# Kernel tuning notes

Measured on AMD Instinct MI355X. Metric: run time of the kernel, lower is better.

Reference implementation:

```python
import jax, jax.numpy as jnp
import numpy as np

S, B, E, H = 2048, 4, 512, 8
D = E // H

# --- Brevitas-style per-tensor fake quantization with straight-through estimator ---

def fq_s8(x):
    """Int8ActPerTensorFloat / Int8WeightPerTensorFloat: symmetric per-tensor abs-max."""
    qmax = 127.0
    scale = jnp.maximum(jnp.max(jnp.abs(x)), 1e-8) / qmax
    q = jnp.clip(jnp.round(x / scale), -128.0, qmax)
    return x + jax.lax.stop_gradient(scale * q - x), scale


def fq_u8(x):
    """Uint8ActPerTensorFloat for attention weights (softmax output, >=0)."""
    qmax = 255.0
    scale = jnp.maximum(jnp.max(x), 1e-8) / qmax
    q = jnp.clip(jnp.round(x / scale), 0.0, qmax)
    return x + jax.lax.stop_gradient(scale * q - x)


def fq_b32(b, scale):
    """Int32Bias: bias quantized with scale = input_scale * weight_scale."""
    qmax = 2.0 ** 31 - 1.0
    q = jnp.clip(jnp.round(b / scale), -qmax, qmax)
    return b + jax.lax.stop_gradient(scale * q - b)


def setup_inputs() -> dict:
    key = jax.random.key(0)
    ks = jax.random.split(key, 9)
    w = lambda k: jax.random.normal(k, (E, E), jnp.float32) * 0.02
    b = lambda k: jax.random.normal(k, (E,), jnp.float32) * 0.02
    return {
        "x": jax.random.normal(ks[0], (S, B, E), jnp.float32),
        "Wq": w(ks[1]), "Wk": w(ks[2]), "Wv": w(ks[3]),
        "bq": b(ks[4]), "bk": b(ks[5]), "bv": b(ks[6]),
        "Wo": w(ks[7]), "bo": b(ks[8]),
    }


def reference(x, Wq, Wk, Wv, bq, bk, bv, Wo, bo):
    # inputQuant (QuantIdentity, int8)
    xq, _ = fq_s8(x)
    # in_proj input quant (int8, per-tensor)
    xi, s_in = fq_s8(xq)

    def proj(W, b_):
        Wf, s_w = fq_s8(W)                    # int8 weight quant
        bf = fq_b32(b_, s_in * s_w)           # int32 bias quant
        return jnp.einsum('sbe,fe->sbf', xi, Wf) + bf

    q = proj(Wq, bq)  # [S,B,E]
    k = proj(Wk, bk)
    v = proj(Wv, bv)

    # split heads: [S,B,E] -> [B,H,S,D]
    heads = lambda t: t.reshape(S, B, H, D).transpose(1, 2, 0, 3)
    q, k, v = heads(q), heads(k), heads(v)

    qs, _ = fq_s8(q / jnp.sqrt(jnp.float32(D)))   # q_scaled_quant (int8)
    kt, _ = fq_s8(k)                              # k_transposed_quant (int8)
    scores = jnp.einsum('bhqd,bhkd->bhqk', qs, kt)  # [B,H,S,S]
    attn = fq_u8(jax.nn.softmax(scores, axis=-1))   # attn_output_weights_quant (uint8)
    vq, _ = fq_s8(v)                                # v_quant (int8)

    ctx = jnp.einsum('bhqk,bhkd->bhqd', attn, vq)   # [B,H,S,D]
    ctx = ctx.transpose(2, 0, 1, 3).reshape(S, B, E)  # back to [S,B,E]

    ci, s_c = fq_s8(ctx)                            # out_proj_input_quant
    Wof, s_wo = fq_s8(Wo)                           # out_proj_weight_quant
    bof = fq_b32(bo, s_c * s_wo)                    # out_proj_bias_quant
    y = jnp.einsum('sbe,fe->sbf', ci, Wof) + bof
    yq, _ = fq_s8(y)                                # out_proj_output_quant
    return yq
```

## Files before the change

### kernel.cpp

```cpp
#include <hip/hip_runtime.h>

constexpr int cS = 2048, cB = 4, cE = 512, cH = 8, cD = 64;
constexpr int cSB = cS * cB;
constexpr int cBH = cB * cH;
constexpr int cN  = cSB * cE;

typedef __bf16 v8bf  __attribute__((ext_vector_type(8)));
typedef float  f32x4 __attribute__((ext_vector_type(4)));

constexpr float cLOG2E = 1.4426950408889634f;


__device__ __forceinline__ unsigned short q2bf(float f) {
  return (unsigned short)(__float_as_uint(f) >> 16);
}
__device__ __forceinline__ float clip8(float t) { return fminf(fmaxf(t, -128.f), 127.f); }
__device__ __forceinline__ float wave_max(float v) {
#pragma unroll
  for (int o = 32; o > 0; o >>= 1) v = fmaxf(v, __shfl_down(v, o));
  return v;
}

__device__ __forceinline__ void stage8k(const unsigned short* __restrict__ gsrc,
                                        unsigned short* lds, int tid) {
  int w = tid >> 6;
#pragma unroll
  for (int is = 0; is < 2; ++is) {
    int c = is * 256 + tid;
    int cp = (c & ~7) | ((c & 7) ^ ((c >> 3) & 7));
    const char* g = (const char*)gsrc + (size_t)cp * 16;
    char* l = (char*)lds + (size_t)(is * 4096 + w * 1024);
    __builtin_amdgcn_global_load_lds(
        (const __attribute__((address_space(1))) unsigned int*)g,
        (__attribute__((address_space(3))) unsigned int*)l, 16, 0, 0);
  }
}
__device__ __forceinline__ v8bf lds_frag(const unsigned short* tile, int row, int chunk) {
  int sc = chunk ^ (row & 7);
  return *(const v8bf*)((const char*)tile + row * 128 + sc * 16);
}

__global__ void absmax_kernel(const float* __restrict__ p, int n4, unsigned* slot) {
  int tid = blockIdx.x * blockDim.x + threadIdx.x, stride = gridDim.x * blockDim.x;
  float m = 0.f;
  for (int i = tid; i < n4; i += stride) {
    float4 v = ((const float4*)p)[i];
    m = fmaxf(m, fmaxf(fmaxf(fabsf(v.x), fabsf(v.y)), fmaxf(fabsf(v.z), fabsf(v.w))));
  }
  m = wave_max(m);
  __shared__ float sm[4];
  int lane = threadIdx.x & 63, wid = threadIdx.x >> 6;
  if (lane == 0) sm[wid] = m;
  __syncthreads();
  if (threadIdx.x == 0) {
    float mm = sm[0];
    for (int w = 1; w < (int)blockDim.x / 64; ++w) mm = fmaxf(mm, sm[w]);
    atomicMax(slot, __float_as_uint(mm));
  }
}

__global__ void absmax4_kernel(const float* __restrict__ w0, const float* __restrict__ w1,
                               const float* __restrict__ w2, const float* __restrict__ w3,
                               int n4, unsigned* slots) {
  int y = blockIdx.y;
  const float* p = (y == 0) ? w0 : (y == 1) ? w1 : (y == 2) ? w2 : w3;
  int tid = blockIdx.x * blockDim.x + threadIdx.x, stride = gridDim.x * blockDim.x;
  float m = 0.f;
  for (int i = tid; i < n4; i += stride) {
    float4 v = ((const float4*)p)[i];
    m = fmaxf(m, fmaxf(fmaxf(fabsf(v.x), fabsf(v.y)), fmaxf(fabsf(v.z), fabsf(v.w))));
  }
  m = wave_max(m);
  __shared__ float sm[4];
  int lane = threadIdx.x & 63, wid = threadIdx.x >> 6;
  if (lane == 0) sm[wid] = m;
  __syncthreads();
  if (threadIdx.x == 0) {
    float mm = fmaxf(fmaxf(sm[0], sm[1]), fmaxf(sm[2], sm[3]));
    atomicMax(slots + y, __float_as_uint(mm));
  }
}

__global__ void scales_kernel(float* st, int stage) {
  if (stage == 0) {
    float s0 = fmaxf(st[0], 1e-8f) / 127.f;
    st[11] = s0;
    float mxq = s0 * 127.f;
    st[12] = fmaxf(mxq, 1e-8f) / 127.f;
    for (int i = 0; i < 4; ++i) st[13 + i] = fmaxf(st[1 + i], 1e-8f) / 127.f;
  } else if (stage == 1) {
    st[17] = fmaxf(st[5] * 0.125f, 1e-8f) / 127.f;
    st[18] = fmaxf(st[6], 1e-8f) / 127.f;
    st[19] = fmaxf(st[7], 1e-8f) / 127.f;
    st[25] = st[17] * st[18];
    st[26] = st[25] * cLOG2E;
  } else if (stage == 2) {
    float sa = fmaxf(st[8], 1e-8f) / 255.f;
    st[20] = sa; st[21] = 1.f / sa; st[22] = sa * st[19];
  } else if (stage == 3) {
    st[23] = fmaxf(st[9], 1e-8f) / 127.f;
  } else {
    st[24] = fmaxf(st[10], 1e-8f) / 127.f;
  }
}

__global__ void quant_x_kernel(const float* __restrict__ x, unsigned short* __restrict__ xq,
                               const float* st, int n4) {
  float s0 = st[11], si = st[12];
  int tid = blockIdx.x * blockDim.x + threadIdx.x, stride = gridDim.x * blockDim.x;
  for (int i = tid; i < n4; i += stride) {
    float4 v = ((const float4*)x)[i];
    ushort4 o; float t;
    t = s0 * clip8(rintf(v.x / s0)); o.x = q2bf(clip8(rintf(t / si)));
    t = s0 * clip8(rintf(v.y / s0)); o.y = q2bf(clip8(rintf(t / si)));
    t = s0 * clip8(rintf(v.z / s0)); o.z = q2bf(clip8(rintf(t / si)));
    t = s0 * clip8(rintf(v.w / s0)); o.w = q2bf(clip8(rintf(t / si)));
    ((ushort4*)xq)[i] = o;
  }
}

__global__ void quant_w4_kernel(const float* __restrict__ w0, const float* __restrict__ w1,
                                const float* __restrict__ w2, const float* __restrict__ w3,
                                unsigned short* __restrict__ outbase, int n4, const float* st) {
  int y = blockIdx.y;
  const float* in = (y == 0) ? w0 : (y == 1) ? w1 : (y == 2) ? w2 : w3;
  unsigned short* outp = outbase + (size_t)y * cE * cE;
  float s = st[13 + y];
  int tid = blockIdx.x * blockDim.x + threadIdx.x, stride = gridDim.x * blockDim.x;
  for (int i = tid; i < n4; i += stride) {
    float4 v = ((const float4*)in)[i];
    ushort4 o;
    o.x = q2bf(clip8(rintf(v.x / s)));
    o.y = q2bf(clip8(rintf(v.y / s)));
    o.z = q2bf(clip8(rintf(v.z / s)));
    o.w = q2bf(clip8(rintf(v.w / s)));
    ((ushort4*)outp)[i] = o;
  }
}

__global__ void quant_s8_kernel(const float* __restrict__ in, unsigned short* __restrict__ outp,
                                int n4, const float* st, int slot, float premul) {
  float s = st[slot];
  int tid = blockIdx.x * blockDim.x + threadIdx.x, stride = gridDim.x * blockDim.x;
  for (int i = tid; i < n4; i += stride) {
    float4 v = ((const float4*)in)[i];
    ushort4 o;
    o.x = q2bf(clip8(rintf(v.x * premul / s)));
    o.y = q2bf(clip8(rintf(v.y * premul / s)));
    o.z = q2bf(clip8(rintf(v.z * premul / s)));
    o.w = q2bf(clip8(rintf(v.w * premul / s)));
    ((ushort4*)outp)[i] = o;
  }
}

__global__ void quant_qk_kernel(const float* __restrict__ qf, unsigned short* __restrict__ qsb,
                                int n4, const float* st) {
  int y = blockIdx.y;
  const float* in = qf + (size_t)y * cN;
  unsigned short* outp = qsb + (size_t)y * cN;
  float s = st[17 + y];
  float premul = y ? 1.0f : 0.125f;
  int tid = blockIdx.x * blockDim.x + threadIdx.x, stride = gridDim.x * blockDim.x;
  for (int i = tid; i < n4; i += stride) {
    float4 v = ((const float4*)in)[i];
    ushort4 o;
    o.x = q2bf(clip8(rintf(v.x * premul / s)));
    o.y = q2bf(clip8(rintf(v.y * premul / s)));
    o.z = q2bf(clip8(rintf(v.z * premul / s)));
    o.w = q2bf(clip8(rintf(v.w * premul / s)));
    ((ushort4*)outp)[i] = o;
  }
}

__global__ void bias3_kernel(const float* __restrict__ b0, const float* __restrict__ b1,
                             const float* __restrict__ b2, float* __restrict__ bdst,
                             const float* st) {
  int y = blockIdx.y;
  const float* bsrc = (y == 0) ? b0 : (y == 1) ? b1 : b2;
  int f = blockIdx.x * blockDim.x + threadIdx.x;
  if (f < cE) {
    float s = st[12] * st[13 + y];
    bdst[y * cE + f] = s * rintf(bsrc[f] / s);
  }
}

__global__ void bias_kernel(const float* __restrict__ bsrc, float* __restrict__ bdst,
                            const float* st, int slot_in, int slot_w) {
  int f = blockIdx.x * blockDim.x + threadIdx.x;
  if (f < cE) {
    float s = st[slot_in] * st[slot_w];
    bdst[f] = s * rintf(bsrc[f] / s);
  }
}

__global__ __launch_bounds__(256) void quant_vT_kernel(const float* __restrict__ v,
                                                       unsigned short* __restrict__ vT,
                                                       const float* st) {
  __shared__ unsigned short tile[64][65];
  int bh = blockIdx.y, bx = blockIdx.x, s0 = bx * 64;
  float sv = st[19];
  int td = threadIdx.x & 63, tr = threadIdx.x >> 6;
  for (int r = tr; r < 64; r += 4)
    tile[r][td] = q2bf(clip8(rintf(v[((size_t)bh * cS + s0 + r) * cD + td] / sv)));
  __syncthreads();
  for (int r = tr; r < 64; r += 4)
    vT[((size_t)(bh * 32 + bx) * 64 + r) * 64 + td] = tile[td][r];
}

__global__ void final_quant_kernel(float* __restrict__ y, const float* st, int n4) {
  float s = st[24];
  int tid = blockIdx.x * blockDim.x + threadIdx.x, stride = gridDim.x * blockDim.x;
  for (int i = tid; i < n4; i += stride) {
    float4 v = ((float4*)y)[i];
    v.x = s * clip8(rintf(v.x / s)); v.y = s * clip8(rintf(v.y / s));
    v.z = s * clip8(rintf(v.z / s)); v.w = s * clip8(rintf(v.w / s));
    ((float4*)y)[i] = v;
  }
}

template <int OUTMODE>
__global__ __launch_bounds__(256) void gemm_kernel(const unsigned short* __restrict__ A,
                                                   const unsigned short* __restrict__ Wb,
                                                   const float* __restrict__ bias,
                                                   float* __restrict__ out, const float* st,
                                                   int slot_in, int slot_w, unsigned* amax_slot) {
  int wid = threadIdx.x >> 6, lane = threadIdx.x & 63;
  int wm = wid >> 1, wn = wid & 1;
  int row0 = blockIdx.x * 64 + wm * 32;
  int col0 = blockIdx.y * 64 + wn * 32;
  int lr = lane & 15, lk = (lane >> 4) * 8;
  f32x4 acc[2][2] = {};
  const unsigned short* a0p = A + (size_t)(row0 + lr) * cE + lk;
  const unsigned short* a1p = A + (size_t)(row0 + 16 + lr) * cE + lk;
  const unsigned short* b0p = Wb + (size_t)(col0 + lr) * cE + lk;
  const unsigned short* b1p = Wb + (size_t)(col0 + 16 + lr) * cE + lk;
  for (int e0 = 0; e0 < cE; e0 += 32) {
    v8bf a0 = *(const v8bf*)(a0p + e0), a1 = *(const v8bf*)(a1p + e0);
    v8bf b0 = *(const v8bf*)(b0p + e0), b1 = *(const v8bf*)(b1p + e0);
    acc[0][0] = __builtin_amdgcn_mfma_f32_16x16x32_bf16(a0, b0, acc[0][0], 0, 0, 0);
    acc[0][1] = __builtin_amdgcn_mfma_f32_16x16x32_bf16(a0, b1, acc[0][1], 0, 0, 0);
    acc[1][0] = __builtin_amdgcn_mfma_f32_16x16x32_bf16(a1, b0, acc[1][0], 0, 0, 0);
    acc[1][1] = __builtin_amdgcn_mfma_f32_16x16x32_bf16(a1, b1, acc[1][1], 0, 0, 0);
  }
  float scale = st[slot_in] * st[slot_w];
  float lmax = 0.f;
#pragma unroll
  for (int mi = 0; mi < 2; ++mi)
#pragma unroll
    for (int ni = 0; ni < 2; ++ni)
#pragma unroll
      for (int r = 0; r < 4; ++r) {
        int row = row0 + mi * 16 + (lane >> 4) * 4 + r;
        int col = col0 + ni * 16 + lr;
        float val = scale * acc[mi][ni][r] + bias[col];
        lmax = fmaxf(lmax, fabsf(val));
        if (OUTMODE == 0) {
          int s = row >> 2, bb = row & 3, h = col >> 6, d = col & 63;
          out[(((size_t)(bb * cH + h)) * cS + s) * cD + d] = val;
        } else {
          out[(size_t)row * cE + col] = val;
        }
      }
  lmax = wave_max(lmax);
  if (lane == 0) atomicMax(amax_slot, __float_as_uint(lmax));
}

__global__ __launch_bounds__(256) void attn_pass1_kernel(const unsigned short* __restrict__ qs,
                                                         const unsigned short* __restrict__ ks,
                                                         float* __restrict__ marr,
                                                         float* __restrict__ izarr,
                                                         const float* st, unsigned* maxiz_slot) {
  __shared__ __align__(16) unsigned short kbuf[2][64][64];
  int tid = threadIdx.x;
  int bh = blockIdx.y;
  int wid = tid >> 6, lane = tid & 63;
  int lr = lane & 15, g = lane >> 4, lk = g * 8;
  int r0 = blockIdx.x * 128 + wid * 32;
  float sscale2 = st[26];
  v8bf aq0[2], aq1[2];
#pragma unroll
  for (int qg = 0; qg < 2; ++qg) {
    const unsigned short* qp = qs + ((size_t)bh * cS + r0 + qg * 16 + lr) * cD + lk;
    aq0[qg] = *(const v8bf*)qp; aq1[qg] = *(const v8bf*)(qp + 32);
  }
  const unsigned short* Kb = ks + (size_t)bh * cS * cD;

  stage8k(Kb, &kbuf[0][0][0], tid);
  __syncthreads();
  float pm[2] = {-1e30f, -1e30f}, zs[2] = {0.f, 0.f};
  int buf = 0;
  for (int t = 0; t < 32; ++t) {
    if (t < 31) stage8k(Kb + (size_t)(t + 1) * 4096, &kbuf[buf ^ 1][0][0], tid);
    const unsigned short* Kt = &kbuf[buf][0][0];
    f32x4 s4[2][4];
#pragma unroll
    for (int jc = 0; jc < 4; ++jc) {
      v8bf k0 = lds_frag(Kt, jc * 16 + lr, g);
      v8bf k1 = lds_frag(Kt, jc * 16 + lr, g + 4);
#pragma unroll
      for (int qg = 0; qg < 2; ++qg) {
        f32x4 z = {0.f, 0.f, 0.f, 0.f};
        z = __builtin_amdgcn_mfma_f32_16x16x32_bf16(k0, aq0[qg], z, 0, 0, 0);
        z = __builtin_amdgcn_mfma_f32_16x16x32_bf16(k1, aq1[qg], z, 0, 0, 0);
        s4[qg][jc] = z;
      }
    }
#pragma unroll
    for (int qg = 0; qg < 2; ++qg) {
      float tv[16];
#pragma unroll
      for (int jc = 0; jc < 4; ++jc)
#pragma unroll
        for (int r = 0; r < 4; ++r) tv[jc * 4 + r] = s4[qg][jc][r] * sscale2;
      float tm = tv[0];
#pragma unroll
      for (int i = 1; i < 16; ++i) tm = fmaxf(tm, tv[i]);
      float nm = fmaxf(pm[qg], tm);
      float acc = zs[qg] * __builtin_amdgcn_exp2f(pm[qg] - nm);
#pragma unroll
      for (int i = 0; i < 16; ++i) acc += __builtin_amdgcn_exp2f(tv[i] - nm);
      zs[qg] = acc; pm[qg] = nm;
    }
    __syncthreads();
    buf ^= 1;
  }
  float wm_l = 0.f;
#pragma unroll
  for (int qg = 0; qg < 2; ++qg) {
    float m = pm[qg], z = zs[qg];
#pragma unroll
    for (int o = 16; o < 64; o <<= 1) {
      float mo = __shfl_xor(m, o);
      float zo = __shfl_xor(z, o);
      float nm = fmaxf(m, mo);
      z = z * __builtin_amdgcn_exp2f(m - nm) + zo * __builtin_amdgcn_exp2f(mo - nm);
      m = nm;
    }
    float iz = 1.0f / z;
    if (g == 0) {
      marr[bh * cS + r0 + qg * 16 + lr] = m;
      izarr[bh * cS + r0 + qg * 16 + lr] = iz;
    }
    wm_l = fmaxf(wm_l, iz);
  }
  float wmax = wave_max(wm_l);
  if (lane == 0) atomicMax(maxiz_slot, __float_as_uint(wmax));
}

__global__ __launch_bounds__(256) void attn_pass2_kernel(
    const unsigned short* __restrict__ qs, const unsigned short* __restrict__ ks,
    const unsigned short* __restrict__ vT, const float* __restrict__ marr,
    const float* __restrict__ izarr, float* __restrict__ ctx, const float* st,
    unsigned* amax_slot) {
  __shared__ __align__(16) unsigned short kbuf[2][64][64];
  __shared__ __align__(16) unsigned short vbuf[2][64][64];
  __shared__ __align__(16) unsigned short plds[4][2][16][88];
  int tid = threadIdx.x;
  int bh = blockIdx.y, b = bh >> 3, h = bh & 7;
  int wid = tid >> 6, lane = tid & 63;
  int lr = lane & 15, g = lane >> 4, lk = g * 8;
  int r0 = blockIdx.x * 128 + wid * 32;
  float sscale2 = st[26], isa = st[21], cscale = st[22];
  v8bf aq0[2], aq1[2];
  float m2[2], fac[2];
#pragma unroll
  for (int qg = 0; qg < 2; ++qg) {
    const unsigned short* qp = qs + ((size_t)bh * cS + r0 + qg * 16 + lr) * cD + lk;
    aq0[qg] = *(const v8bf*)qp; aq1[qg] = *(const v8bf*)(qp + 32);
    m2[qg] = marr[bh * cS + r0 + qg * 16 + lr];
    fac[qg] = izarr[bh * cS + r0 + qg * 16 + lr] * isa;
  }
  const unsigned short* Kb = ks + (size_t)bh * cS * cD;
  const unsigned short* Vb = vT + (size_t)bh * 32 * 4096;
  f32x4 cacc[2][4] = {};

  stage8k(Kb, &kbuf[0][0][0], tid);
  stage8k(Vb, &vbuf[0][0][0], tid);
  __syncthreads();
  int buf = 0;
  for (int t = 0; t < 32; ++t) {
    if (t < 31) {
      stage8k(Kb + (size_t)(t + 1) * 4096, &kbuf[buf ^ 1][0][0], tid);
      stage8k(Vb + (size_t)(t + 1) * 4096, &vbuf[buf ^ 1][0][0], tid);
    }
    const unsigned short* Kt = &kbuf[buf][0][0];
    const unsigned short* Vt = &vbuf[buf][0][0];
#pragma unroll
    for (int jc = 0; jc < 4; ++jc) {
      v8bf k0 = lds_frag(Kt, jc * 16 + lr, g);
      v8bf k1 = lds_frag(Kt, jc * 16 + lr, g + 4);
#pragma unroll
      for (int qg = 0; qg < 2; ++qg) {
        f32x4 z = {0.f, 0.f, 0.f, 0.f};
        z = __builtin_amdgcn_mfma_f32_16x16x32_bf16(k0, aq0[qg], z, 0, 0, 0);
        z = __builtin_amdgcn_mfma_f32_16x16x32_bf16(k1, aq1[qg], z, 0, 0, 0);
        float a0 = fminf(rintf(__builtin_amdgcn_exp2f(__builtin_fmaf(z[0], sscale2, -m2[qg])) * fac[qg]), 255.f);
        float a1 = fminf(rintf(__builtin_amdgcn_exp2f(__builtin_fmaf(z[1], sscale2, -m2[qg])) * fac[qg]), 255.f);
        float a2 = fminf(rintf(__builtin_amdgcn_exp2f(__builtin_fmaf(z[2], sscale2, -m2[qg])) * fac[qg]), 255.f);
        float a3 = fminf(rintf(__builtin_amdgcn_exp2f(__builtin_fmaf(z[3], sscale2, -m2[qg])) * fac[qg]), 255.f);
        uint2 pw;
        pw.x = (__float_as_uint(a0) >> 16) | (__float_as_uint(a1) & 0xFFFF0000u);
        pw.y = (__float_as_uint(a2) >> 16) | (__float_as_uint(a3) & 0xFFFF0000u);
        *(uint2*)&plds[wid][qg][lr][jc * 16 + g * 4] = pw;
      }
    }
    v8bf ap0[2], ap1[2];
#pragma unroll
    for (int qg = 0; qg < 2; ++qg) {
      ap0[qg] = *(const v8bf*)&plds[wid][qg][lr][lk];
      ap1[qg] = *(const v8bf*)&plds[wid][qg][lr][32 + lk];
    }
#pragma unroll
    for (int dt = 0; dt < 4; ++dt) {
      v8bf v0 = lds_frag(Vt, dt * 16 + lr, g);
      v8bf v1 = lds_frag(Vt, dt * 16 + lr, g + 4);
#pragma unroll
      for (int qg = 0; qg < 2; ++qg) {
        cacc[qg][dt] = __builtin_amdgcn_mfma_f32_16x16x32_bf16(ap0[qg], v0, cacc[qg][dt], 0, 0, 0);
        cacc[qg][dt] = __builtin_amdgcn_mfma_f32_16x16x32_bf16(ap1[qg], v1, cacc[qg][dt], 0, 0, 0);
      }
    }
    __syncthreads();
    buf ^= 1;
  }
  float lmax = 0.f;
#pragma unroll
  for (int qg = 0; qg < 2; ++qg)
#pragma unroll
    for (int dt = 0; dt < 4; ++dt)
#pragma unroll
      for (int r = 0; r < 4; ++r) {
        int qrow = r0 + qg * 16 + g * 4 + r;
        int d = dt * 16 + lr;
        float val = cscale * cacc[qg][dt][r];
        lmax = fmaxf(lmax, fabsf(val));
        ctx[((size_t)qrow * cB + b) * cE + h * cD + d] = val;
      }
  lmax = wave_max(lmax);
  if (lane == 0) atomicMax(amax_slot, __float_as_uint(lmax));
}

extern "C" void kernel_launch(void* const* d_in, const int* in_sizes, int n_in, void* d_out,
                              int out_size, void* d_ws, size_t ws_size, hipStream_t stream) {
  (void)in_sizes; (void)n_in; (void)out_size; (void)ws_size;
  const float* x  = (const float*)d_in[0];
  const float* Wq = (const float*)d_in[1];
  const float* Wk = (const float*)d_in[2];
  const float* Wv = (const float*)d_in[3];
  const float* bq = (const float*)d_in[4];
  const float* bk = (const float*)d_in[5];
  const float* bv = (const float*)d_in[6];
  const float* Wo = (const float*)d_in[7];
  const float* bo = (const float*)d_in[8];
  float* out = (float*)d_out;

  char* ws = (char*)d_ws;
  size_t off = 0;
  auto alloc = [&](size_t bytes) { size_t o = off; off += (bytes + 255) & ~(size_t)255; return o; };
  float* st = (float*)(ws + alloc(64 * 4));
  unsigned short* xq  = (unsigned short*)(ws + alloc((size_t)cN * 2));
  unsigned short* wbq = (unsigned short*)(ws + alloc((size_t)cE * cE * 2));
  unsigned short* wbk = (unsigned short*)(ws + alloc((size_t)cE * cE * 2));
  unsigned short* wbv = (unsigned short*)(ws + alloc((size_t)cE * cE * 2));
  unsigned short* wbo = (unsigned short*)(ws + alloc((size_t)cE * cE * 2));
  float* bfq = (float*)(ws + alloc(cE * 4));
  float* bfk = (float*)(ws + alloc(cE * 4));
  float* bfv = (float*)(ws + alloc(cE * 4));
  float* bfo = (float*)(ws + alloc(cE * 4));
  float* qf = (float*)(ws + alloc((size_t)cN * 4));
  float* kf = (float*)(ws + alloc((size_t)cN * 4));
  float* vf = (float*)(ws + alloc((size_t)cN * 4));
  unsigned short* qsb = (unsigned short*)(ws + alloc((size_t)cN * 2));
  unsigned short* ksb = (unsigned short*)(ws + alloc((size_t)cN * 2));
  unsigned short* vTb = (unsigned short*)(ws + alloc((size_t)cN * 2));
  float* marr  = (float*)(ws + alloc((size_t)cBH * cS * 4));
  float* izarr = (float*)(ws + alloc((size_t)cBH * cS * 4));
  float* ctxf = qf;
  unsigned short* cib = (unsigned short*)kf;

  int n4 = cN / 4;
  int nw4 = cE * cE / 4;
  hipMemsetAsync(st, 0, 256, stream);
  absmax_kernel<<<1024, 256, 0, stream>>>(x, n4, (unsigned*)(st + 0));
  absmax4_kernel<<<dim3(64, 4), 256, 0, stream>>>(Wq, Wk, Wv, Wo, nw4, (unsigned*)(st + 1));
  scales_kernel<<<1, 1, 0, stream>>>(st, 0);
  quant_x_kernel<<<1024, 256, 0, stream>>>(x, xq, st, n4);
  quant_w4_kernel<<<dim3(64, 4), 256, 0, stream>>>(Wq, Wk, Wv, Wo, wbq, nw4, st);
  bias3_kernel<<<dim3(2, 3), 256, 0, stream>>>(bq, bk, bv, bfq, st);
  gemm_kernel<0><<<dim3(cSB / 64, cE / 64), 256, 0, stream>>>(xq, wbq, bfq, qf, st, 12, 13, (unsigned*)(st + 5));
  gemm_kernel<0><<<dim3(cSB / 64, cE / 64), 256, 0, stream>>>(xq, wbk, bfk, kf, st, 12, 14, (unsigned*)(st + 6));
  gemm_kernel<0><<<dim3(cSB / 64, cE / 64), 256, 0, stream>>>(xq, wbv, bfv, vf, st, 12, 15, (unsigned*)(st + 7));
  scales_kernel<<<1, 1, 0, stream>>>(st, 1);
  quant_qk_kernel<<<dim3(512, 2), 256, 0, stream>>>(qf, qsb, n4, st);
  quant_vT_kernel<<<dim3(cS / 64, cBH), 256, 0, stream>>>(vf, vTb, st);
  attn_pass1_kernel<<<dim3(cS / 128, cBH), 256, 0, stream>>>(qsb, ksb, marr, izarr, st, (unsigned*)(st + 8));
  scales_kernel<<<1, 1, 0, stream>>>(st, 2);
  attn_pass2_kernel<<<dim3(cS / 128, cBH), 256, 0, stream>>>(qsb, ksb, vTb, marr, izarr, ctxf, st, (unsigned*)(st + 9));
  scales_kernel<<<1, 1, 0, stream>>>(st, 3);
  quant_s8_kernel<<<1024, 256, 0, stream>>>(ctxf, cib, n4, st, 23, 1.0f);
  bias_kernel<<<2, 256, 0, stream>>>(bo, bfo, st, 23, 16);
  gemm_kernel<1><<<dim3(cSB / 64, cE / 64), 256, 0, stream>>>(cib, wbo, bfo, out, st, 23, 16, (unsigned*)(st + 10));
  scales_kernel<<<1, 1, 0, stream>>>(st, 4);
  final_quant_kernel<<<1024, 256, 0, stream>>>(out, st, n4);
}
```

Measured before the change: 535.0 us.

## Fuse QKV projections into one GEMM launch with LDS staging and drop scale kernels

Removes the five single-thread scales kernels and instead recomputes each quantization scale inline from the raw absmax slots inside every consumer kernel. It also merges the three Q/K/V projection GEMMs into one 24-column-block launch. The GEMM is rewritten to double-buffer swizzled 64x64 A/B tiles in LDS via global_load_lds instead of reading fragments straight from global memory. The aim is to cut launch count and serialization and to improve operand reuse in the GEMMs. The cost is a little redundant scalar math per thread and more LDS use. The fused launch relies on the K and V output buffers lying contiguously after qf, and the bias and weight buffers lying contiguously too.

```diff
diff --git a/kernel.cpp b/kernel.cpp
--- a/kernel.cpp
+++ b/kernel.cpp
@@ -15,6 +15,7 @@
   return (unsigned short)(__float_as_uint(f) >> 16);
 }
 __device__ __forceinline__ float clip8(float t) { return fminf(fmaxf(t, -128.f), 127.f); }
+__device__ __forceinline__ float sc127(float amax) { return fmaxf(amax, 1e-8f) / 127.f; }
 __device__ __forceinline__ float wave_max(float v) {
 #pragma unroll
   for (int o = 32; o > 0; o >>= 1) v = fmaxf(v, __shfl_down(v, o));
@@ -29,6 +30,21 @@
     int c = is * 256 + tid;
     int cp = (c & ~7) | ((c & 7) ^ ((c >> 3) & 7));
     const char* g = (const char*)gsrc + (size_t)cp * 16;
+    char* l = (char*)lds + (size_t)(is * 4096 + w * 1024);
+    __builtin_amdgcn_global_load_lds(
+        (const __attribute__((address_space(1))) unsigned int*)g,
+        (__attribute__((address_space(3))) unsigned int*)l, 16, 0, 0);
+  }
+}
+__device__ __forceinline__ void stage_rows(const unsigned short* __restrict__ g0,
+                                           unsigned short* lds, int tid) {
+  int w = tid >> 6;
+#pragma unroll
+  for (int is = 0; is < 2; ++is) {
+    int c = is * 256 + tid;
+    int row = c >> 3;
+    int kc = (c & 7) ^ (row & 7);
+    const char* g = (const char*)(g0 + (size_t)row * cE + kc * 8);
     char* l = (char*)lds + (size_t)(is * 4096 + w * 1024);
     __builtin_amdgcn_global_load_lds(
         (const __attribute__((address_space(1))) unsigned int*)g,
@@ -81,32 +97,10 @@
   }
 }
 
-__global__ void scales_kernel(float* st, int stage) {
-  if (stage == 0) {
-    float s0 = fmaxf(st[0], 1e-8f) / 127.f;
-    st[11] = s0;
-    float mxq = s0 * 127.f;
-    st[12] = fmaxf(mxq, 1e-8f) / 127.f;
-    for (int i = 0; i < 4; ++i) st[13 + i] = fmaxf(st[1 + i], 1e-8f) / 127.f;
-  } else if (stage == 1) {
-    st[17] = fmaxf(st[5] * 0.125f, 1e-8f) / 127.f;
-    st[18] = fmaxf(st[6], 1e-8f) / 127.f;
-    st[19] = fmaxf(st[7], 1e-8f) / 127.f;
-    st[25] = st[17] * st[18];
-    st[26] = st[25] * cLOG2E;
-  } else if (stage == 2) {
-    float sa = fmaxf(st[8], 1e-8f) / 255.f;
-    st[20] = sa; st[21] = 1.f / sa; st[22] = sa * st[19];
-  } else if (stage == 3) {
-    st[23] = fmaxf(st[9], 1e-8f) / 127.f;
-  } else {
-    st[24] = fmaxf(st[10], 1e-8f) / 127.f;
-  }
-}
-
 __global__ void quant_x_kernel(const float* __restrict__ x, unsigned short* __restrict__ xq,
                                const float* st, int n4) {
-  float s0 = st[11], si = st[12];
+  float s0 = sc127(st[0]);
+  float si = fmaxf(s0 * 127.f, 1e-8f) / 127.f;
   int tid = blockIdx.x * blockDim.x + threadIdx.x, stride = gridDim.x * blockDim.x;
   for (int i = tid; i < n4; i += stride) {
     float4 v = ((const float4*)x)[i];
@@ -125,7 +119,7 @@
   int y = blockIdx.y;
   const float* in = (y == 0) ? w0 : (y == 1) ? w1 : (y == 2) ? w2 : w3;
   unsigned short* outp = outbase + (size_t)y * cE * cE;
-  float s = st[13 + y];
+  float s = sc127(st[1 + y]);
   int tid = blockIdx.x * blockDim.x + threadIdx.x, stride = gridDim.x * blockDim.x;
   for (int i = tid; i < n4; i += stride) {
     float4 v = ((const float4*)in)[i];
@@ -138,9 +132,28 @@
   }
 }
 
-__global__ void quant_s8_kernel(const float* __restrict__ in, unsigned short* __restrict__ outp,
-                                int n4, const float* st, int slot, float premul) {
-  float s = st[slot];
+__global__ void quant_ctx_kernel(const float* __restrict__ in, unsigned short* __restrict__ outp,
+                                 int n4, const float* st) {
+  float s = sc127(st[9]);
+  int tid = blockIdx.x * blockDim.x + threadIdx.x, stride = gridDim.x * blockDim.x;
+  for (int i = tid; i < n4; i += stride) {
+    float4 v = ((const float4*)in)[i];
+    ushort4 o;
+    o.x = q2bf(clip8(rintf(v.x / s)));
+    o.y = q2bf(clip8(rintf(v.y / s)));
+    o.z = q2bf(clip8(rintf(v.z / s)));
+    o.w = q2bf(clip8(rintf(v.w / s)));
+    ((ushort4*)outp)[i] = o;
+  }
+}
+
+__global__ void quant_qk_kernel(const float* __restrict__ qf, unsigned short* __restrict__ qsb,
+                                int n4, const float* st) {
+  int y = blockIdx.y;
+  const float* in = qf + (size_t)y * cN;
+  unsigned short* outp = qsb + (size_t)y * cN;
+  float s = y ? sc127(st[6]) : (fmaxf(st[5] * 0.125f, 1e-8f) / 127.f);
+  float premul = y ? 1.0f : 0.125f;
   int tid = blockIdx.x * blockDim.x + threadIdx.x, stride = gridDim.x * blockDim.x;
   for (int i = tid; i < n4; i += stride) {
     float4 v = ((const float4*)in)[i];
@@ -153,25 +166,6 @@
   }
 }
 
-__global__ void quant_qk_kernel(const float* __restrict__ qf, unsigned short* __restrict__ qsb,
-                                int n4, const float* st) {
-  int y = blockIdx.y;
-  const float* in = qf + (size_t)y * cN;
-  unsigned short* outp = qsb + (size_t)y * cN;
-  float s = st[17 + y];
-  float premul = y ? 1.0f : 0.125f;
-  int tid = blockIdx.x * blockDim.x + threadIdx.x, stride = gridDim.x * blockDim.x;
-  for (int i = tid; i < n4; i += stride) {
-    float4 v = ((const float4*)in)[i];
-    ushort4 o;
-    o.x = q2bf(clip8(rintf(v.x * premul / s)));
-    o.y = q2bf(clip8(rintf(v.y * premul / s)));
-    o.z = q2bf(clip8(rintf(v.z * premul / s)));
-    o.w = q2bf(clip8(rintf(v.w * premul / s)));
-    ((ushort4*)outp)[i] = o;
-  }
-}
-
 __global__ void bias3_kernel(const float* __restrict__ b0, const float* __restrict__ b1,
                              const float* __restrict__ b2, float* __restrict__ bdst,
                              const float* st) {
@@ -179,16 +173,18 @@
   const float* bsrc = (y == 0) ? b0 : (y == 1) ? b1 : b2;
   int f = blockIdx.x * blockDim.x + threadIdx.x;
   if (f < cE) {
-    float s = st[12] * st[13 + y];
+    float s0 = sc127(st[0]);
+    float si = fmaxf(s0 * 127.f, 1e-8f) / 127.f;
+    float s = si * sc127(st[1 + y]);
     bdst[y * cE + f] = s * rintf(bsrc[f] / s);
   }
 }
 
-__global__ void bias_kernel(const float* __restrict__ bsrc, float* __restrict__ bdst,
-                            const float* st, int slot_in, int slot_w) {
+__global__ void bias_o_kernel(const float* __restrict__ bsrc, float* __restrict__ bdst,
+                              const float* st) {
   int f = blockIdx.x * blockDim.x + threadIdx.x;
   if (f < cE) {
-    float s = st[slot_in] * st[slot_w];
+    float s = sc127(st[9]) * sc127(st[4]);
     bdst[f] = s * rintf(bsrc[f] / s);
   }
 }
@@ -198,7 +194,7 @@
                                                        const float* st) {
   __shared__ unsigned short tile[64][65];
   int bh = blockIdx.y, bx = blockIdx.x, s0 = bx * 64;
-  float sv = st[19];
+  float sv = sc127(st[7]);
   int td = threadIdx.x & 63, tr = threadIdx.x >> 6;
   for (int r = tr; r < 64; r += 4)
     tile[r][td] = q2bf(clip8(rintf(v[((size_t)bh * cS + s0 + r) * cD + td] / sv)));
@@ -208,7 +204,7 @@
 }
 
 __global__ void final_quant_kernel(float* __restrict__ y, const float* st, int n4) {
-  float s = st[24];
+  float s = sc127(st[10]);
   int tid = blockIdx.x * blockDim.x + threadIdx.x, stride = gridDim.x * blockDim.x;
   for (int i = tid; i < n4; i += stride) {
     float4 v = ((float4*)y)[i];
@@ -218,31 +214,67 @@
   }
 }
 
-template <int OUTMODE>
+template <int MODE>
 __global__ __launch_bounds__(256) void gemm_kernel(const unsigned short* __restrict__ A,
-                                                   const unsigned short* __restrict__ Wb,
-                                                   const float* __restrict__ bias,
-                                                   float* __restrict__ out, const float* st,
-                                                   int slot_in, int slot_w, unsigned* amax_slot) {
-  int wid = threadIdx.x >> 6, lane = threadIdx.x & 63;
+                                                   const unsigned short* __restrict__ Wbase,
+                                                   const float* __restrict__ biasbase,
+                                                   float* __restrict__ outbase, const float* st,
+                                                   unsigned* amax_base) {
+  __shared__ __align__(16) unsigned short abuf[2][64][64];
+  __shared__ __align__(16) unsigned short bbuf[2][64][64];
+  int tid = threadIdx.x, wid = tid >> 6, lane = tid & 63;
   int wm = wid >> 1, wn = wid & 1;
-  int row0 = blockIdx.x * 64 + wm * 32;
-  int col0 = blockIdx.y * 64 + wn * 32;
-  int lr = lane & 15, lk = (lane >> 4) * 8;
+  int lr = lane & 15, g = lane >> 4;
+  int row0 = blockIdx.x * 64;
+  int wsel = (MODE == 0) ? (blockIdx.y >> 3) : 0;
+  int col0 = (MODE == 0) ? ((blockIdx.y & 7) * 64) : (blockIdx.y * 64);
+
+  float scale;
+  float* out;
+  const float* bias;
+  unsigned* amax_slot;
+  if (MODE == 0) {
+    float s0 = sc127(st[0]);
+    float si = fmaxf(s0 * 127.f, 1e-8f) / 127.f;
+    scale = si * sc127(st[1 + wsel]);
+    out = outbase + (size_t)wsel * cN;
+    bias = biasbase + wsel * cE;
+    amax_slot = amax_base + wsel;
+  } else {
+    scale = sc127(st[9]) * sc127(st[4]);
+    out = outbase;
+    bias = biasbase;
+    amax_slot = amax_base;
+  }
+  const unsigned short* Ab = A + (size_t)row0 * cE;
+  const unsigned short* Bb = Wbase + (size_t)wsel * cE * cE + (size_t)col0 * cE;
+
+  stage_rows(Ab, &abuf[0][0][0], tid);
+  stage_rows(Bb, &bbuf[0][0][0], tid);
+  __syncthreads();
   f32x4 acc[2][2] = {};
-  const unsigned short* a0p = A + (size_t)(row0 + lr) * cE + lk;
-  const unsigned short* a1p = A + (size_t)(row0 + 16 + lr) * cE + lk;
-  const unsigned short* b0p = Wb + (size_t)(col0 + lr) * cE + lk;
-  const unsigned short* b1p = Wb + (size_t)(col0 + 16 + lr) * cE + lk;
-  for (int e0 = 0; e0 < cE; e0 += 32) {
-    v8bf a0 = *(const v8bf*)(a0p + e0), a1 = *(const v8bf*)(a1p + e0);
-    v8bf b0 = *(const v8bf*)(b0p + e0), b1 = *(const v8bf*)(b1p + e0);
-    acc[0][0] = __builtin_amdgcn_mfma_f32_16x16x32_bf16(a0, b0, acc[0][0], 0, 0, 0);
-    acc[0][1] = __builtin_amdgcn_mfma_f32_16x16x32_bf16(a0, b1, acc[0][1], 0, 0, 0);
-    acc[1][0] = __builtin_amdgcn_mfma_f32_16x16x32_bf16(a1, b0, acc[1][0], 0, 0, 0);
-    acc[1][1] = __builtin_amdgcn_mfma_f32_16x16x32_bf16(a1, b1, acc[1][1], 0, 0, 0);
-  }
-  float scale = st[slot_in] * st[slot_w];
+  int buf = 0;
+  for (int kt = 0; kt < 8; ++kt) {
+    if (kt < 7) {
+      stage_rows(Ab + (kt + 1) * 64, &abuf[buf ^ 1][0][0], tid);
+      stage_rows(Bb + (kt + 1) * 64, &bbuf[buf ^ 1][0][0], tid);
+    }
+    const unsigned short* At = &abuf[buf][0][0];
+    const unsigned short* Bt = &bbuf[buf][0][0];
+#pragma unroll
+    for (int e = 0; e < 2; ++e) {
+      v8bf a0 = lds_frag(At, wm * 32 + lr, e * 4 + g);
+      v8bf a1 = lds_frag(At, wm * 32 + 16 + lr, e * 4 + g);
+      v8bf b0 = lds_frag(Bt, wn * 32 + lr, e * 4 + g);
+      v8bf b1 = lds_frag(Bt, wn * 32 + 16 + lr, e * 4 + g);
+      acc[0][0] = __builtin_amdgcn_mfma_f32_16x16x32_bf16(a0, b0, acc[0][0], 0, 0, 0);
+      acc[0][1] = __builtin_amdgcn_mfma_f32_16x16x32_bf16(a0, b1, acc[0][1], 0, 0, 0);
+      acc[1][0] = __builtin_amdgcn_mfma_f32_16x16x32_bf16(a1, b0, acc[1][0], 0, 0, 0);
+      acc[1][1] = __builtin_amdgcn_mfma_f32_16x16x32_bf16(a1, b1, acc[1][1], 0, 0, 0);
+    }
+    __syncthreads();
+    buf ^= 1;
+  }
   float lmax = 0.f;
 #pragma unroll
   for (int mi = 0; mi < 2; ++mi)
@@ -250,11 +282,11 @@
     for (int ni = 0; ni < 2; ++ni)
 #pragma unroll
       for (int r = 0; r < 4; ++r) {
-        int row = row0 + mi * 16 + (lane >> 4) * 4 + r;
-        int col = col0 + ni * 16 + lr;
+        int row = row0 + wm * 32 + mi * 16 + g * 4 + r;
+        int col = col0 + wn * 32 + ni * 16 + lr;
         float val = scale * acc[mi][ni][r] + bias[col];
         lmax = fmaxf(lmax, fabsf(val));
-        if (OUTMODE == 0) {
+        if (MODE == 0) {
           int s = row >> 2, bb = row & 3, h = col >> 6, d = col & 63;
           out[(((size_t)(bb * cH + h)) * cS + s) * cD + d] = val;
         } else {
@@ -276,7 +308,9 @@
   int wid = tid >> 6, lane = tid & 63;
   int lr = lane & 15, g = lane >> 4, lk = g * 8;
   int r0 = blockIdx.x * 128 + wid * 32;
-  float sscale2 = st[26];
+  float sq = fmaxf(st[5] * 0.125f, 1e-8f) / 127.f;
+  float sk = sc127(st[6]);
+  float sscale2 = (sq * sk) * cLOG2E;
   v8bf aq0[2], aq1[2];
 #pragma unroll
   for (int qg = 0; qg < 2; ++qg) {
@@ -360,7 +394,12 @@
   int wid = tid >> 6, lane = tid & 63;
   int lr = lane & 15, g = lane >> 4, lk = g * 8;
   int r0 = blockIdx.x * 128 + wid * 32;
-  float sscale2 = st[26], isa = st[21], cscale = st[22];
+  float sq = fmaxf(st[5] * 0.125f, 1e-8f) / 127.f;
+  float sk = sc127(st[6]);
+  float sscale2 = (sq * sk) * cLOG2E;
+  float sa = fmaxf(st[8], 1e-8f) / 255.f;
+  float isa = 1.f / sa;
+  float cscale = sa * sc127(st[7]);
   v8bf aq0[2], aq1[2];
   float m2[2], fac[2];
 #pragma unroll
@@ -480,26 +519,20 @@
 
   int n4 = cN / 4;
   int nw4 = cE * cE / 4;
+  (void)kf; (void)vf; (void)bfk; (void)bfv;
   hipMemsetAsync(st, 0, 256, stream);
   absmax_kernel<<<1024, 256, 0, stream>>>(x, n4, (unsigned*)(st + 0));
   absmax4_kernel<<<dim3(64, 4), 256, 0, stream>>>(Wq, Wk, Wv, Wo, nw4, (unsigned*)(st + 1));
-  scales_kernel<<<1, 1, 0, stream>>>(st, 0);
   quant_x_kernel<<<1024, 256, 0, stream>>>(x, xq, st, n4);
   quant_w4_kernel<<<dim3(64, 4), 256, 0, stream>>>(Wq, Wk, Wv, Wo, wbq, nw4, st);
   bias3_kernel<<<dim3(2, 3), 256, 0, stream>>>(bq, bk, bv, bfq, st);
-  gemm_kernel<0><<<dim3(cSB / 64, cE / 64), 256, 0, stream>>>(xq, wbq, bfq, qf, st, 12, 13, (unsigned*)(st + 5));
-  gemm_kernel<0><<<dim3(cSB / 64, cE / 64), 256, 0, stream>>>(xq, wbk, bfk, kf, st, 12, 14, (unsigned*)(st + 6));
-  gemm_kernel<0><<<dim3(cSB / 64, cE / 64), 256, 0, stream>>>(xq, wbv, bfv, vf, st, 12, 15, (unsigned*)(st + 7));
-  scales_kernel<<<1, 1, 0, stream>>>(st, 1);
+  gemm_kernel<0><<<dim3(cSB / 64, 24), 256, 0, stream>>>(xq, wbq, bfq, qf, st, (unsigned*)(st + 5));
   quant_qk_kernel<<<dim3(512, 2), 256, 0, stream>>>(qf, qsb, n4, st);
   quant_vT_kernel<<<dim3(cS / 64, cBH), 256, 0, stream>>>(vf, vTb, st);
   attn_pass1_kernel<<<dim3(cS / 128, cBH), 256, 0, stream>>>(qsb, ksb, marr, izarr, st, (unsigned*)(st + 8));
-  scales_kernel<<<1, 1, 0, stream>>>(st, 2);
   attn_pass2_kernel<<<dim3(cS / 128, cBH), 256, 0, stream>>>(qsb, ksb, vTb, marr, izarr, ctxf, st, (unsigned*)(st + 9));
-  scales_kernel<<<1, 1, 0, stream>>>(st, 3);
-  quant_s8_kernel<<<1024, 256, 0, stream>>>(ctxf, cib, n4, st, 23, 1.0f);
-  bias_kernel<<<2, 256, 0, stream>>>(bo, bfo, st, 23, 16);
-  gemm_kernel<1><<<dim3(cSB / 64, cE / 64), 256, 0, stream>>>(cib, wbo, bfo, out, st, 23, 16, (unsigned*)(st + 10));
-  scales_kernel<<<1, 1, 0, stream>>>(st, 4);
+  quant_ctx_kernel<<<1024, 256, 0, stream>>>(ctxf, cib, n4, st);
+  bias_o_kernel<<<2, 256, 0, stream>>>(bo, bfo, st);
+  gemm_kernel<1><<<dim3(cSB / 64, cE / 64), 256, 0, stream>>>(cib, wbo, bfo, out, st, (unsigned*)(st + 10));
   final_quant_kernel<<<1024, 256, 0, stream>>>(out, st, n4);
 }
```

Measured after the change: 485.5 us. -9.2%, faster.
